# Kernel optimization log

Measured on AMD Instinct MI355X. Metric: run time of the kernel, lower is better.

Reference implementation:

```python
import jax, jax.numpy as jnp
import numpy as np

B, S, D, H = 4, 2048, 512, 8
DK = D // H


def setup_inputs() -> dict:
    key = jax.random.key(0)
    ks = jax.random.split(key, 11)
    scale = 1.0 / np.sqrt(D)
    inp = {
        'q': jax.random.normal(ks[0], (B, S, D), jnp.float32),
        'k': jax.random.normal(ks[1], (B, S, D), jnp.float32),
        'v': jax.random.normal(ks[2], (B, S, D), jnp.float32),
        'mask': jnp.tril(jnp.ones((S, S), jnp.int32))[None, None, :, :],  # [1,1,S,S] causal
        'w_q': jax.random.normal(ks[3], (D, D), jnp.float32) * scale,
        'b_q': jnp.zeros((D,), jnp.float32),
        'w_k': jax.random.normal(ks[4], (D, D), jnp.float32) * scale,
        'b_k': jnp.zeros((D,), jnp.float32),
        'w_v': jax.random.normal(ks[5], (D, D), jnp.float32) * scale,
        'b_v': jnp.zeros((D,), jnp.float32),
        'w_o': jax.random.normal(ks[6], (D, D), jnp.float32) * scale,
        'b_o': jnp.zeros((D,), jnp.float32),
    }
    return inp


def reference(q, k, v, mask, w_q, b_q, w_k, b_k, w_v, b_v, w_o, b_o):
    # QKV projections (nn.Linear: x @ W^T + b)
    def split_heads(x):  # [B,S,D] -> [B,H,S,DK]
        return x.reshape(B, S, H, DK).transpose(0, 2, 1, 3)

    qh = split_heads(q @ w_q.T + b_q)
    kh = split_heads(k @ w_k.T + b_k)
    vh = split_heads(v @ w_v.T + b_v)

    scores = jnp.einsum('bhqd,bhkd->bhqk', qh, kh) / jnp.sqrt(jnp.float32(DK))
    scores = jnp.where(mask == 0, jnp.float32(-1e9), scores)
    attn = jax.nn.softmax(scores, axis=-1)  # dropout is identity in eval
    ctx = jnp.einsum('bhqk,bhkd->bhqd', attn, vh)  # [B,H,S,DK]
    ctx = ctx.transpose(0, 2, 1, 3).reshape(B, S, D)
    return ctx @ w_o.T + b_o
```

## Files before the change

kernel.cpp:

```cpp
#include <hip/hip_runtime.h>
#include <hip/hip_bf16.h>


#define BATCH  4
#define SLEN   2048
#define DMODEL 512
#define NHEAD  8
#define DHEAD  64
#define MROWS  (BATCH * SLEN)

#define NQ ((size_t)MROWS * DMODEL)
#define NW ((size_t)DMODEL * DMODEL)
#define NB ((size_t)DMODEL)
#define CVTW_TOTAL (4 * NW + 4 * NB)

#define SCALE_L2E 0.180336880f

typedef short bf16x8 __attribute__((ext_vector_type(8)));
typedef float f32x4  __attribute__((ext_vector_type(4)));

typedef unsigned int __attribute__((address_space(1))) glb_u32_t;
typedef unsigned int __attribute__((address_space(3))) lds_u32_t;

__device__ __forceinline__ void async16(const void* g, void* l) {
    __builtin_amdgcn_global_load_lds((glb_u32_t*)g, (lds_u32_t*)l, 16, 0, 0);
}

__device__ __forceinline__ float bf2f(unsigned short u) {
    union { unsigned int i; float f; } v; v.i = ((unsigned int)u) << 16; return v.f;
}
__device__ __forceinline__ unsigned short f2bf(float f) {
    union { float f; unsigned int i; } v; v.f = f;
    unsigned int x = v.i;
    return (unsigned short)((x + 0x7fffu + ((x >> 16) & 1u)) >> 16);
}
__device__ __forceinline__ unsigned int pkbf(float a, float b) {
    union { __hip_bfloat162 h; unsigned int u; } cv;
    cv.h = __float22bfloat162_rn(float2{a, b});
    return cv.u;
}

__device__ __forceinline__ void wait0_barrier() {
    asm volatile("s_waitcnt vmcnt(0)" ::: "memory");
    __builtin_amdgcn_s_barrier();
    asm volatile("" ::: "memory");
}

__global__ __launch_bounds__(256)
void cvt_w_kernel(const float* __restrict__ wq, const float* __restrict__ wk,
                  const float* __restrict__ wv, const float* __restrict__ wo,
                  const float* __restrict__ bq, const float* __restrict__ bk,
                  const float* __restrict__ bv, const float* __restrict__ bo,
                  unsigned short* __restrict__ dst)
{
    const size_t i4 = ((size_t)blockIdx.x * 256 + threadIdx.x) * 4;
    if (i4 >= CVTW_TOTAL) return;
    const float* src;
    size_t off;
    if      (i4 <     NW)          { src = wq; off = i4; }
    else if (i4 < 2 * NW)          { src = wk; off = i4 - NW; }
    else if (i4 < 3 * NW)          { src = wv; off = i4 - 2 * NW; }
    else if (i4 < 4 * NW)          { src = wo; off = i4 - 3 * NW; }
    else if (i4 < 4 * NW + NB)     { src = bq; off = i4 - 4 * NW; }
    else if (i4 < 4 * NW + 2 * NB) { src = bk; off = i4 - 4 * NW - NB; }
    else if (i4 < 4 * NW + 3 * NB) { src = bv; off = i4 - 4 * NW - 2 * NB; }
    else                           { src = bo; off = i4 - 4 * NW - 3 * NB; }
    const float4 f = *(const float4*)(src + off);
    ushort4 o;
    o.x = f2bf(f.x); o.y = f2bf(f.y); o.z = f2bf(f.z); o.w = f2bf(f.w);
    *(ushort4*)(dst + i4) = o;
}

__device__ __forceinline__ void qkv_body(const float* __restrict__ A,
                                         const unsigned short* __restrict__ W,
                                         const unsigned short* __restrict__ bias,
                                         unsigned short* __restrict__ C,
                                         int mode, int m0, int n0,
                                         unsigned char* smem)
{
    float*          Asf = (float*)smem;
    unsigned short* Bs  = (unsigned short*)(smem + 32768);

    const int tid  = threadIdx.x;
    const int wave = tid >> 6;
    const int lane = tid & 63;
    const int l15  = lane & 15;
    const int quad = lane >> 4;
    const int wm   = (wave & 1) * 64;
    const int wn   = (wave >> 1) * 64;
    const int srow = lane >> 2;
    const int scol = (((lane & 3) ^ (srow & 3)) * 8);
    const int rswb = (quad ^ (l15 & 3)) * 8;
    const int krow = lane >> 3;
    const int acol = ((lane & 7) ^ (krow & 7)) * 4;

    auto stageA = [&](int k0, int buf) {
        #pragma unroll
        for (int c = 0; c < 4; c++) {
            const int rb = c * 32 + wave * 8;
            async16(A + (size_t)(m0 + rb + krow) * DMODEL + k0 + acol,
                    Asf + (size_t)buf * 4096 + rb * 32);
        }
    };
    auto stageW = [&](int k0, int buf) {
        async16(W + (size_t)(n0 + wave * 16 + srow) * DMODEL + k0 + scol,
                Bs + (size_t)buf * 4096 + wave * 512);
        async16(W + (size_t)(n0 + (wave + 4) * 16 + srow) * DMODEL + k0 + scol,
                Bs + (size_t)buf * 4096 + (wave + 4) * 512);
    };

    f32x4 acc[4][4] = {};
    stageA(0, 0);
    stageW(0, 0);

    #pragma unroll 1
    for (int kt = 0; kt < 16; kt++) {
        const int cur = kt & 1;
        wait0_barrier();
        if (kt < 15) { stageA((kt + 1) * 32, cur ^ 1); stageW((kt + 1) * 32, cur ^ 1); }

        bf16x8 af[4], bfr[4];
        #pragma unroll
        for (int i = 0; i < 4; i++) {
            const int row = wm + i * 16 + l15;
            const float* rp = Asf + (size_t)cur * 4096 + row * 32;
            const f32x4 x = *(const f32x4*)(rp + (((quad * 2)     ^ (row & 7)) * 4));
            const f32x4 y = *(const f32x4*)(rp + (((quad * 2 + 1) ^ (row & 7)) * 4));
            union { bf16x8 v; unsigned int u[4]; } r;
            r.u[0] = pkbf(x[0], x[1]); r.u[1] = pkbf(x[2], x[3]);
            r.u[2] = pkbf(y[0], y[1]); r.u[3] = pkbf(y[2], y[3]);
            af[i] = r.v;
        }
        #pragma unroll
        for (int j = 0; j < 4; j++)
            bfr[j] = *(const bf16x8*)(Bs + (size_t)cur * 4096 + (wn + j * 16 + l15) * 32 + rswb);
        #pragma unroll
        for (int i = 0; i < 4; i++)
            #pragma unroll
            for (int j = 0; j < 4; j++)
                acc[i][j] = __builtin_amdgcn_mfma_f32_16x16x32_bf16(af[i], bfr[j], acc[i][j], 0, 0, 0);
    }

    if (mode == 2) {
        #pragma unroll
        for (int j = 0; j < 4; j++) {
            const int col = n0 + wn + j * 16 + l15;
            const float bv = bf2f(bias[col]);
            const int hh = col >> 6, dk = col & 63;
            #pragma unroll
            for (int i = 0; i < 4; i++) {
                const int row = m0 + wm + i * 16 + quad * 4;
                const int bb = row >> 11, s = row & 2047;
                uint2 o2;
                o2.x = pkbf(acc[i][j][0] + bv, acc[i][j][1] + bv);
                o2.y = pkbf(acc[i][j][2] + bv, acc[i][j][3] + bv);
                *(uint2*)(C + ((size_t)((bb * NHEAD + hh) * DHEAD + dk)) * SLEN + s) = o2;
            }
        }
    } else {
        const float oscale = (mode == 0) ? SCALE_L2E : 1.0f;
        #pragma unroll
        for (int j = 0; j < 4; j++) {
            const int col = n0 + wn + j * 16 + l15;
            const float bv = bf2f(bias[col]);
            #pragma unroll
            for (int i = 0; i < 4; i++) {
                const int row = m0 + wm + i * 16 + quad * 4;
                #pragma unroll
                for (int r = 0; r < 4; r++)
                    C[(size_t)(row + r) * DMODEL + col] = f2bf((acc[i][j][r] + bv) * oscale);
            }
        }
    }
}

__global__ __launch_bounds__(256, 3)
void qkv_gemm_kernel(const float* __restrict__ qin, const float* __restrict__ kin,
                     const float* __restrict__ vin,
                     const unsigned short* __restrict__ wq, const unsigned short* __restrict__ bq,
                     const unsigned short* __restrict__ wk, const unsigned short* __restrict__ bk,
                     const unsigned short* __restrict__ wv, const unsigned short* __restrict__ bv,
                     unsigned short* __restrict__ qh, unsigned short* __restrict__ kh,
                     unsigned short* __restrict__ vt)
{
    __shared__ __align__(16) unsigned char smem[49152];
    const int z = blockIdx.z;
    const float*          A    = (z == 0) ? qin : (z == 1) ? kin : vin;
    const unsigned short* W    = (z == 0) ? wq  : (z == 1) ? wk  : wv;
    const unsigned short* bias = (z == 0) ? bq  : (z == 1) ? bk  : bv;
    unsigned short*       C    = (z == 0) ? qh  : (z == 1) ? kh  : vt;
    qkv_body(A, W, bias, C, z, blockIdx.x * 128, blockIdx.y * 128, smem);
}

__device__ __forceinline__ void attn_body(const unsigned short* __restrict__ qh,
                                          const unsigned short* __restrict__ kh,
                                          const unsigned short* __restrict__ vt,
                                          unsigned short* __restrict__ ctx,
                                          int bh, int qt, unsigned char* smem)
{
    unsigned short* Ks = (unsigned short*)smem;
    unsigned short* Vs = Ks + 2 * 64 * 64;
    unsigned short* Ps = Vs + 2 * 64 * 64;

    const int tid  = threadIdx.x;
    const int wave = tid >> 6;
    const int lane = tid & 63;
    const int l15  = lane & 15;
    const int quad = lane >> 4;
    const int b = bh >> 3, h = bh & 7;

    const size_t base = (size_t)b * SLEN * DMODEL + (size_t)h * DHEAD;
    const unsigned short* Q  = qh + base;
    const unsigned short* K  = kh + base;
    const unsigned short* VT = vt + (size_t)bh * DHEAD * SLEN;

    const int krow_l = lane >> 3;
    const int kcol_l = ((lane & 7) ^ (krow_l & 7)) * 8;

    const int qrow = qt * 64 + wave * 16 + l15;
    const bf16x8 qf0 = *(const bf16x8*)(Q + (size_t)qrow * DMODEL + quad * 8);
    const bf16x8 qf1 = *(const bf16x8*)(Q + (size_t)qrow * DMODEL + 32 + quad * 8);

    f32x4 oacc[4] = {};
    float lsum = 0.0f;
    unsigned short* Pw = Ps + wave * (16 * 64);
    const int ktiles = qt + 1;

    auto stageKV = [&](int kt, int buf) {
        async16(K + (size_t)(kt * 64 + wave * 8 + krow_l) * DMODEL + kcol_l,
                Ks + (size_t)buf * 4096 + wave * 512);
        async16(K + (size_t)(kt * 64 + (wave + 4) * 8 + krow_l) * DMODEL + kcol_l,
                Ks + (size_t)buf * 4096 + (wave + 4) * 512);
        async16(VT + (size_t)(wave * 8 + krow_l) * SLEN + kt * 64 + kcol_l,
                Vs + (size_t)buf * 4096 + wave * 512);
        async16(VT + (size_t)((wave + 4) * 8 + krow_l) * SLEN + kt * 64 + kcol_l,
                Vs + (size_t)buf * 4096 + (wave + 4) * 512);
    };

    stageKV(0, 0);

    #pragma unroll 1
    for (int kt = 0; kt < ktiles; kt++) {
        const int cur = kt & 1;
        wait0_barrier();
        if (kt + 1 < ktiles) stageKV(kt + 1, cur ^ 1);

        f32x4 sacc[4] = {};
        #pragma unroll
        for (int kk = 0; kk < 2; kk++) {
            const bf16x8 qf = kk ? qf1 : qf0;
            #pragma unroll
            for (int j = 0; j < 4; j++) {
                bf16x8 kf = *(const bf16x8*)(Ks + (size_t)cur * 4096 + (j * 16 + l15) * 64
                                                + (((kk * 4 + quad) ^ (l15 & 7)) * 8));
                sacc[j] = __builtin_amdgcn_mfma_f32_16x16x32_bf16(kf, qf, sacc[j], 0, 0, 0);
            }
        }

        if (kt == qt) {
            #pragma unroll
            for (int j = 0; j < 4; j++)
                #pragma unroll
                for (int r = 0; r < 4; r++) {
                    const int kv = kt * 64 + j * 16 + quad * 4 + r;
                    if (kv > qrow) sacc[j][r] = -1e30f;
                }
        }

        #pragma unroll
        for (int j = 0; j < 4; j++) {
            const float p0 = exp2f(sacc[j][0]);
            const float p1 = exp2f(sacc[j][1]);
            const float p2v = exp2f(sacc[j][2]);
            const float p3 = exp2f(sacc[j][3]);
            lsum += (p0 + p1) + (p2v + p3);
            uint2 pw;
            pw.x = pkbf(p0, p1);
            pw.y = pkbf(p2v, p3);
            const int chunk = (j * 2 + (quad >> 1)) ^ (l15 & 7);
            *(uint2*)(Pw + l15 * 64 + chunk * 8 + (quad & 1) * 4) = pw;
        }
        asm volatile("s_waitcnt lgkmcnt(0)" ::: "memory");

        #pragma unroll
        for (int kk = 0; kk < 2; kk++) {
            bf16x8 pf = *(const bf16x8*)(Pw + l15 * 64 + (((kk * 4 + quad) ^ (l15 & 7)) * 8));
            #pragma unroll
            for (int jd = 0; jd < 4; jd++) {
                bf16x8 vf = *(const bf16x8*)(Vs + (size_t)cur * 4096 + (jd * 16 + l15) * 64
                                                + (((kk * 4 + quad) ^ (l15 & 7)) * 8));
                oacc[jd] = __builtin_amdgcn_mfma_f32_16x16x32_bf16(vf, pf, oacc[jd], 0, 0, 0);
            }
        }
    }

    lsum += __shfl_xor(lsum, 16, 64);
    lsum += __shfl_xor(lsum, 32, 64);
    const float invl = 1.0f / lsum;

    #pragma unroll
    for (int jd = 0; jd < 4; jd++) {
        uint2 o2;
        o2.x = pkbf(oacc[jd][0] * invl, oacc[jd][1] * invl);
        o2.y = pkbf(oacc[jd][2] * invl, oacc[jd][3] * invl);
        *(uint2*)(ctx + base + (size_t)qrow * DMODEL + jd * 16 + quad * 4) = o2;
    }
}

__global__ __launch_bounds__(256, 4)
void attn_kernel(const unsigned short* __restrict__ qh,
                 const unsigned short* __restrict__ kh,
                 const unsigned short* __restrict__ vt,
                 unsigned short* __restrict__ ctx)
{
    __shared__ __align__(16) unsigned char smem[40960];
    const int bh = blockIdx.x;
    const int x  = blockIdx.y;
    const int g  = x & 7, s = x >> 3;
    const int qt = (s == 0) ? g : (s == 1) ? 15 - g : (s == 2) ? 16 + g : 31 - g;
    attn_body(qh, kh, vt, ctx, bh, qt, smem);
}

__device__ __forceinline__ void oproj_body(const unsigned short* __restrict__ ctx,
                                           const unsigned short* __restrict__ wo,
                                           const unsigned short* __restrict__ bo,
                                           float* __restrict__ out,
                                           int m0, int n0, unsigned char* smem)
{
    unsigned short* As = (unsigned short*)smem;
    unsigned short* Bs = As + 2 * 64 * 32;

    const int tid  = threadIdx.x;
    const int wave = tid >> 6;
    const int lane = tid & 63;
    const int l15  = lane & 15;
    const int quad = lane >> 4;
    const int wm   = (wave & 1) * 32;
    const int wn   = (wave >> 1) * 32;
    const int srow = lane >> 2;
    const int scol = (((lane & 3) ^ (srow & 3)) * 8);
    const int rsw  = (quad ^ (l15 & 3)) * 8;

    auto stage = [&](int k0, int buf) {
        async16(ctx + (size_t)(m0 + wave * 16 + srow) * DMODEL + k0 + scol,
                As + (size_t)buf * 2048 + wave * 512);
        async16(wo + (size_t)(n0 + wave * 16 + srow) * DMODEL + k0 + scol,
                Bs + (size_t)buf * 2048 + wave * 512);
    };

    f32x4 acc[2][2] = {};
    stage(0, 0);

    #pragma unroll 1
    for (int kt = 0; kt < 16; kt++) {
        const int cur = kt & 1;
        wait0_barrier();
        if (kt < 15) stage((kt + 1) * 32, cur ^ 1);

        bf16x8 af[2], bfr[2];
        #pragma unroll
        for (int i = 0; i < 2; i++)
            af[i] = *(const bf16x8*)(As + (size_t)cur * 2048 + (wm + i * 16 + l15) * 32 + rsw);
        #pragma unroll
        for (int j = 0; j < 2; j++)
            bfr[j] = *(const bf16x8*)(Bs + (size_t)cur * 2048 + (wn + j * 16 + l15) * 32 + rsw);
        #pragma unroll
        for (int i = 0; i < 2; i++)
            #pragma unroll
            for (int j = 0; j < 2; j++)
                acc[i][j] = __builtin_amdgcn_mfma_f32_16x16x32_bf16(af[i], bfr[j], acc[i][j], 0, 0, 0);
    }

    #pragma unroll
    for (int j = 0; j < 2; j++) {
        const int col = n0 + wn + j * 16 + l15;
        const float bv = bf2f(bo[col]);
        #pragma unroll
        for (int i = 0; i < 2; i++) {
            const int row = m0 + wm + i * 16 + quad * 4;
            #pragma unroll
            for (int r = 0; r < 4; r++)
                out[(size_t)(row + r) * DMODEL + col] = acc[i][j][r] + bv;
        }
    }
}

__global__ __launch_bounds__(256, 4)
void oproj_gemm_kernel(const unsigned short* __restrict__ ctx,
                       const unsigned short* __restrict__ wo,
                       const unsigned short* __restrict__ bo,
                       float* __restrict__ out)
{
    __shared__ __align__(16) unsigned char smem[16384];
    oproj_body(ctx, wo, bo, out, blockIdx.x * 64, blockIdx.y * 64, smem);
}

extern "C" void kernel_launch(void* const* d_in, const int* in_sizes, int n_in,
                              void* d_out, int out_size, void* d_ws, size_t ws_size,
                              hipStream_t stream)
{
    const float* q   = (const float*)d_in[0];
    const float* k   = (const float*)d_in[1];
    const float* v   = (const float*)d_in[2];
    const float* w_q = (const float*)d_in[4];
    const float* b_q = (const float*)d_in[5];
    const float* w_k = (const float*)d_in[6];
    const float* b_k = (const float*)d_in[7];
    const float* w_v = (const float*)d_in[8];
    const float* b_v = (const float*)d_in[9];
    const float* w_o = (const float*)d_in[10];
    const float* b_o = (const float*)d_in[11];
    float* out = (float*)d_out;
    unsigned short* ws = (unsigned short*)d_ws;

    unsigned short* wqb = ws + 3 * NQ;
    unsigned short* wkb = wqb + NW;
    unsigned short* wvb = wkb + NW;
    unsigned short* wob = wvb + NW;
    unsigned short* bqb = wob + NW;
    unsigned short* bkb = bqb + NB;
    unsigned short* bvb = bkb + NB;
    unsigned short* bob = bvb + NB;
    unsigned short* qh  = bob + NB;
    unsigned short* kh  = qh + NQ;
    unsigned short* vt  = kh + NQ;
    unsigned short* ctx = vt + NQ;

    dim3 blk(256);
    hipLaunchKernelGGL(cvt_w_kernel, dim3((unsigned)(CVTW_TOTAL / 4 / 256)), blk, 0, stream,
                       w_q, w_k, w_v, w_o, b_q, b_k, b_v, b_o, wqb);
    hipLaunchKernelGGL(qkv_gemm_kernel, dim3(MROWS / 128, DMODEL / 128, 3), blk, 0, stream,
                       q, k, v, wqb, bqb, wkb, bkb, wvb, bvb, qh, kh, vt);
    hipLaunchKernelGGL(attn_kernel, dim3(BATCH * NHEAD, 32), blk, 0, stream,
                       qh, kh, vt, ctx);
    hipLaunchKernelGGL(oproj_gemm_kernel, dim3(MROWS / 64, DMODEL / 64), blk, 0, stream,
                       ctx, wob, bob, out);
}
```

Measured before the change: 194.0 us.

## Use 32x32 MFMA with 128-row query tiles in attention kernel

The attention kernel now gives each wave 32 query rows instead of 16, so a block covers 128 query rows, and it switches from 16x16x32 to 32x32x16 bf16 MFMA instructions. This halves the grid and doubles the reuse of each staged K/V tile across query rows, cutting K/V traffic and LDS reads per FLOP. Causal masking now applies on the last two key tiles. In exchange, register and LDS use per block rise, occupancy drops (launch bounds go from 4 to 2), and fewer blocks give coarser load balancing across the causal triangle.

Measured after the change: 206.6 us. 1.07x slower.

```diff
diff --git a/kernel.cpp b/kernel.cpp
--- a/kernel.cpp
+++ b/kernel.cpp
@@ -16,8 +16,9 @@
 
 #define SCALE_L2E 0.180336880f
 
-typedef short bf16x8 __attribute__((ext_vector_type(8)));
-typedef float f32x4  __attribute__((ext_vector_type(4)));
+typedef short bf16x8  __attribute__((ext_vector_type(8)));
+typedef float f32x4   __attribute__((ext_vector_type(4)));
+typedef float f32x16  __attribute__((ext_vector_type(16)));
 
 typedef unsigned int __attribute__((address_space(1))) glb_u32_t;
 typedef unsigned int __attribute__((address_space(3))) lds_u32_t;
@@ -192,133 +193,131 @@
     qkv_body(A, W, bias, C, z, blockIdx.x * 128, blockIdx.y * 128, smem);
 }
 
-__device__ __forceinline__ void attn_body(const unsigned short* __restrict__ qh,
-                                          const unsigned short* __restrict__ kh,
-                                          const unsigned short* __restrict__ vt,
-                                          unsigned short* __restrict__ ctx,
-                                          int bh, int qt, unsigned char* smem)
-{
-    unsigned short* Ks = (unsigned short*)smem;
-    unsigned short* Vs = Ks + 2 * 64 * 64;
-    unsigned short* Ps = Vs + 2 * 64 * 64;
-
-    const int tid  = threadIdx.x;
-    const int wave = tid >> 6;
-    const int lane = tid & 63;
-    const int l15  = lane & 15;
-    const int quad = lane >> 4;
-    const int b = bh >> 3, h = bh & 7;
-
-    const size_t base = (size_t)b * SLEN * DMODEL + (size_t)h * DHEAD;
-    const unsigned short* Q  = qh + base;
-    const unsigned short* K  = kh + base;
-    const unsigned short* VT = vt + (size_t)bh * DHEAD * SLEN;
-
-    const int krow_l = lane >> 3;
-    const int kcol_l = ((lane & 7) ^ (krow_l & 7)) * 8;
-
-    const int qrow = qt * 64 + wave * 16 + l15;
-    const bf16x8 qf0 = *(const bf16x8*)(Q + (size_t)qrow * DMODEL + quad * 8);
-    const bf16x8 qf1 = *(const bf16x8*)(Q + (size_t)qrow * DMODEL + 32 + quad * 8);
-
-    f32x4 oacc[4] = {};
-    float lsum = 0.0f;
-    unsigned short* Pw = Ps + wave * (16 * 64);
-    const int ktiles = qt + 1;
-
-    auto stageKV = [&](int kt, int buf) {
-        async16(K + (size_t)(kt * 64 + wave * 8 + krow_l) * DMODEL + kcol_l,
-                Ks + (size_t)buf * 4096 + wave * 512);
-        async16(K + (size_t)(kt * 64 + (wave + 4) * 8 + krow_l) * DMODEL + kcol_l,
-                Ks + (size_t)buf * 4096 + (wave + 4) * 512);
-        async16(VT + (size_t)(wave * 8 + krow_l) * SLEN + kt * 64 + kcol_l,
-                Vs + (size_t)buf * 4096 + wave * 512);
-        async16(VT + (size_t)((wave + 4) * 8 + krow_l) * SLEN + kt * 64 + kcol_l,
-                Vs + (size_t)buf * 4096 + (wave + 4) * 512);
-    };
-
-    stageKV(0, 0);
-
-    #pragma unroll 1
-    for (int kt = 0; kt < ktiles; kt++) {
-        const int cur = kt & 1;
-        wait0_barrier();
-        if (kt + 1 < ktiles) stageKV(kt + 1, cur ^ 1);
-
-        f32x4 sacc[4] = {};
-        #pragma unroll
-        for (int kk = 0; kk < 2; kk++) {
-            const bf16x8 qf = kk ? qf1 : qf0;
-            #pragma unroll
-            for (int j = 0; j < 4; j++) {
-                bf16x8 kf = *(const bf16x8*)(Ks + (size_t)cur * 4096 + (j * 16 + l15) * 64
-                                                + (((kk * 4 + quad) ^ (l15 & 7)) * 8));
-                sacc[j] = __builtin_amdgcn_mfma_f32_16x16x32_bf16(kf, qf, sacc[j], 0, 0, 0);
-            }
-        }
-
-        if (kt == qt) {
-            #pragma unroll
-            for (int j = 0; j < 4; j++)
-                #pragma unroll
-                for (int r = 0; r < 4; r++) {
-                    const int kv = kt * 64 + j * 16 + quad * 4 + r;
-                    if (kv > qrow) sacc[j][r] = -1e30f;
-                }
-        }
-
-        #pragma unroll
-        for (int j = 0; j < 4; j++) {
-            const float p0 = exp2f(sacc[j][0]);
-            const float p1 = exp2f(sacc[j][1]);
-            const float p2v = exp2f(sacc[j][2]);
-            const float p3 = exp2f(sacc[j][3]);
-            lsum += (p0 + p1) + (p2v + p3);
-            uint2 pw;
-            pw.x = pkbf(p0, p1);
-            pw.y = pkbf(p2v, p3);
-            const int chunk = (j * 2 + (quad >> 1)) ^ (l15 & 7);
-            *(uint2*)(Pw + l15 * 64 + chunk * 8 + (quad & 1) * 4) = pw;
-        }
-        asm volatile("s_waitcnt lgkmcnt(0)" ::: "memory");
-
-        #pragma unroll
-        for (int kk = 0; kk < 2; kk++) {
-            bf16x8 pf = *(const bf16x8*)(Pw + l15 * 64 + (((kk * 4 + quad) ^ (l15 & 7)) * 8));
-            #pragma unroll
-            for (int jd = 0; jd < 4; jd++) {
-                bf16x8 vf = *(const bf16x8*)(Vs + (size_t)cur * 4096 + (jd * 16 + l15) * 64
-                                                + (((kk * 4 + quad) ^ (l15 & 7)) * 8));
-                oacc[jd] = __builtin_amdgcn_mfma_f32_16x16x32_bf16(vf, pf, oacc[jd], 0, 0, 0);
-            }
-        }
-    }
-
-    lsum += __shfl_xor(lsum, 16, 64);
-    lsum += __shfl_xor(lsum, 32, 64);
-    const float invl = 1.0f / lsum;
-
-    #pragma unroll
-    for (int jd = 0; jd < 4; jd++) {
-        uint2 o2;
-        o2.x = pkbf(oacc[jd][0] * invl, oacc[jd][1] * invl);
-        o2.y = pkbf(oacc[jd][2] * invl, oacc[jd][3] * invl);
-        *(uint2*)(ctx + base + (size_t)qrow * DMODEL + jd * 16 + quad * 4) = o2;
-    }
-}
-
-__global__ __launch_bounds__(256, 4)
+__global__ __launch_bounds__(256, 2)
 void attn_kernel(const unsigned short* __restrict__ qh,
                  const unsigned short* __restrict__ kh,
                  const unsigned short* __restrict__ vt,
                  unsigned short* __restrict__ ctx)
 {
-    __shared__ __align__(16) unsigned char smem[40960];
+    __shared__ __align__(16) unsigned short Ks[2][64 * 64];
+    __shared__ __align__(16) unsigned short Vs[2][64 * 64];
+    __shared__ __align__(16) unsigned short Ps[4][32 * 64];
+
+    const int tid  = threadIdx.x;
+    const int wave = tid >> 6;
+    const int lane = tid & 63;
+    const int l31  = lane & 31;
+    const int hi   = lane >> 5;
+
     const int bh = blockIdx.x;
     const int x  = blockIdx.y;
-    const int g  = x & 7, s = x >> 3;
-    const int qt = (s == 0) ? g : (s == 1) ? 15 - g : (s == 2) ? 16 + g : 31 - g;
-    attn_body(qh, kh, vt, ctx, bh, qt, smem);
+    const int qt = (x < 8) ? 15 - x : x - 8;
+    const int b  = bh >> 3;
+    const int hd = bh & 7;
+
+    const size_t base = (size_t)b * SLEN * DMODEL + (size_t)hd * DHEAD;
+    const unsigned short* Q  = qh + base;
+    const unsigned short* K  = kh + base;
+    const unsigned short* VT = vt + (size_t)bh * DHEAD * SLEN;
+
+    const int krow_l = lane >> 3;
+    const int kcol_l = ((lane & 7) ^ (krow_l & 7)) * 8;
+
+    const int qrow = qt * 128 + wave * 32 + l31;
+    bf16x8 qf[4];
+    #pragma unroll
+    for (int d = 0; d < 4; d++)
+        qf[d] = *(const bf16x8*)(Q + (size_t)qrow * DMODEL + d * 16 + hi * 8);
+
+    f32x16 oacc[2] = {};
+    float lsum = 0.0f;
+    unsigned short* Pw = &Ps[wave][0];
+    const int nkt = 2 * qt + 2;
+
+    auto stageKV = [&](int kt, int buf) {
+        async16(K + (size_t)(kt * 64 + wave * 8 + krow_l) * DMODEL + kcol_l,
+                &Ks[buf][0] + wave * 512);
+        async16(K + (size_t)(kt * 64 + (wave + 4) * 8 + krow_l) * DMODEL + kcol_l,
+                &Ks[buf][0] + (wave + 4) * 512);
+        async16(VT + (size_t)(wave * 8 + krow_l) * SLEN + kt * 64 + kcol_l,
+                &Vs[buf][0] + wave * 512);
+        async16(VT + (size_t)((wave + 4) * 8 + krow_l) * SLEN + kt * 64 + kcol_l,
+                &Vs[buf][0] + (wave + 4) * 512);
+    };
+
+    stageKV(0, 0);
+
+    #pragma unroll 1
+    for (int kt = 0; kt < nkt; kt++) {
+        const int cur = kt & 1;
+        wait0_barrier();
+        if (kt + 1 < nkt) stageKV(kt + 1, cur ^ 1);
+
+        f32x16 sacc[2] = {};
+        #pragma unroll
+        for (int d = 0; d < 4; d++) {
+            #pragma unroll
+            for (int s = 0; s < 2; s++) {
+                bf16x8 kf = *(const bf16x8*)(&Ks[cur][0] + (s * 32 + l31) * 64
+                                                + (((d * 2 + hi) ^ (l31 & 7)) * 8));
+                sacc[s] = __builtin_amdgcn_mfma_f32_32x32x16_bf16(kf, qf[d], sacc[s], 0, 0, 0);
+            }
+        }
+
+        if (kt * 64 + 63 > qrow) {
+            #pragma unroll
+            for (int s = 0; s < 2; s++)
+                #pragma unroll
+                for (int r = 0; r < 16; r++) {
+                    const int kv = kt * 64 + s * 32 + (r & 3) + 8 * (r >> 2) + 4 * hi;
+                    if (kv > qrow) sacc[s][r] = -1e30f;
+                }
+        }
+
+        #pragma unroll
+        for (int s = 0; s < 2; s++) {
+            #pragma unroll
+            for (int m = 0; m < 4; m++) {
+                const float p0 = exp2f(sacc[s][4 * m + 0]);
+                const float p1 = exp2f(sacc[s][4 * m + 1]);
+                const float p2 = exp2f(sacc[s][4 * m + 2]);
+                const float p3 = exp2f(sacc[s][4 * m + 3]);
+                lsum += (p0 + p1) + (p2 + p3);
+                uint2 pw;
+                pw.x = pkbf(p0, p1);
+                pw.y = pkbf(p2, p3);
+                const int chunk = (s * 4 + m) ^ (l31 & 7);
+                *(uint2*)(Pw + l31 * 64 + chunk * 8 + hi * 4) = pw;
+            }
+        }
+        asm volatile("s_waitcnt lgkmcnt(0)" ::: "memory");
+
+        #pragma unroll
+        for (int kk = 0; kk < 4; kk++) {
+            bf16x8 pf = *(const bf16x8*)(Pw + l31 * 64 + (((kk * 2 + hi) ^ (l31 & 7)) * 8));
+            #pragma unroll
+            for (int t = 0; t < 2; t++) {
+                bf16x8 vf = *(const bf16x8*)(&Vs[cur][0] + (t * 32 + l31) * 64
+                                                + (((kk * 2 + hi) ^ (l31 & 7)) * 8));
+                oacc[t] = __builtin_amdgcn_mfma_f32_32x32x16_bf16(vf, pf, oacc[t], 0, 0, 0);
+            }
+        }
+    }
+
+    lsum += __shfl_xor(lsum, 32, 64);
+    const float invl = 1.0f / lsum;
+
+    #pragma unroll
+    for (int t = 0; t < 2; t++) {
+        #pragma unroll
+        for (int m = 0; m < 4; m++) {
+            const int d0 = t * 32 + 8 * m + 4 * hi;
+            uint2 o2;
+            o2.x = pkbf(oacc[t][4 * m + 0] * invl, oacc[t][4 * m + 1] * invl);
+            o2.y = pkbf(oacc[t][4 * m + 2] * invl, oacc[t][4 * m + 3] * invl);
+            *(uint2*)(ctx + base + (size_t)qrow * DMODEL + d0) = o2;
+        }
+    }
 }
 
 __device__ __forceinline__ void oproj_body(const unsigned short* __restrict__ ctx,
@@ -431,7 +430,7 @@
                        w_q, w_k, w_v, w_o, b_q, b_k, b_v, b_o, wqb);
     hipLaunchKernelGGL(qkv_gemm_kernel, dim3(MROWS / 128, DMODEL / 128, 3), blk, 0, stream,
                        q, k, v, wqb, bqb, wkb, bkb, wvb, bvb, qh, kh, vt);
-    hipLaunchKernelGGL(attn_kernel, dim3(BATCH * NHEAD, 32), blk, 0, stream,
+    hipLaunchKernelGGL(attn_kernel, dim3(BATCH * NHEAD, 16), blk, 0, stream,
                        qh, kh, vt, ctx);
     hipLaunchKernelGGL(oproj_gemm_kernel, dim3(MROWS / 64, DMODEL / 64), blk, 0, stream,
                        ctx, wob, bob, out);
```
